# Optimization experiments

Hardware: AMD Instinct MI355X
Metric: run time of the kernel (lower is better)

## Reference

```python
import jax, jax.numpy as jnp
import numpy as np

TYPE_PANEL, TYPE_DIALOG, TYPE_CHAR = 1, 2, 3
NUM_ELEMS = 64  # max element index per type (panel count cap per page)
B, S, D = 8, 4096, 768
NPC, NDS = 4, 4  # num_panel_classes, num_dialog_shapes


def setup_inputs() -> dict:
    key = jax.random.key(0)
    ks = jax.random.split(key, 16)
    w = lambda k, shp: jax.random.normal(k, shp, dtype=jnp.float32) * 0.02
    return {
        "element_types": jax.random.randint(ks[0], (B, S), 0, 4, dtype=jnp.int32),
        "element_indices": jax.random.randint(ks[1], (B, S), 0, NUM_ELEMS, dtype=jnp.int32),
        "parent_panel_indices": jax.random.randint(ks[2], (B, S), 0, NUM_ELEMS, dtype=jnp.int32),
        "style_vector": jax.random.normal(ks[3], (B, 4), dtype=jnp.float32),
        "type_emb": w(ks[4], (4, D)),
        "index_emb": w(ks[5], (NUM_ELEMS, D)),
        "parent_emb": w(ks[6], (NUM_ELEMS, D)),
        "style_w": w(ks[7], (4, D)),
        "style_b": jnp.zeros((D,), jnp.float32),
        "ln_g": jnp.ones((D,), jnp.float32),
        "ln_b": jnp.zeros((D,), jnp.float32),
        "panel_w": w(ks[8], (D, NPC + 4)),
        "panel_b": jnp.zeros((NPC + 4,), jnp.float32),
        "dialog_w": w(ks[9], (2 * D, NDS + 4)),
        "dialog_b": jnp.zeros((NDS + 4,), jnp.float32),
        "char_w": w(ks[10], (2 * D, 4)),
        "char_b": jnp.zeros((4,), jnp.float32),
    }


def reference(element_types, element_indices, parent_panel_indices, style_vector,
              type_emb, index_emb, parent_emb, style_w, style_b, ln_g, ln_b,
              panel_w, panel_b, dialog_w, dialog_b, char_w, char_b):
    Bv, Sv = element_types.shape
    # --- TokenLayoutEncoder: embedding sum + style projection + LayerNorm ---
    x = type_emb[element_types] + index_emb[element_indices] + parent_emb[parent_panel_indices]
    x = x + (style_vector @ style_w + style_b)[:, None, :]
    mu = x.mean(-1, keepdims=True)
    var = ((x - mu) ** 2).mean(-1, keepdims=True)
    feats = (x - mu) * jax.lax.rsqrt(var + 1e-5) * ln_g + ln_b  # (B,S,D)

    # --- vectorized _build_parent_remap: orig panel idx -> kept panel order pos ---
    panel_mask = element_types == TYPE_PANEL                      # (B,S)
    kept = (jnp.cumsum(panel_mask, axis=1) - 1).astype(jnp.int32) # order pos of each panel token
    brow = jnp.arange(Bv, dtype=jnp.int32)[:, None]
    col = jnp.where(panel_mask, element_indices, NUM_ELEMS)       # dummy slot for non-panels
    remap = (jnp.full((Bv, NUM_ELEMS + 1), -1, jnp.int32)
             .at[brow, col].max(kept))[:, :NUM_ELEMS]             # (B, NUM_ELEMS)
    # kept panel order pos -> sequence position (for parent feature gather)
    slot = jnp.where(panel_mask, kept, Sv)
    seq_ids = jnp.broadcast_to(jnp.arange(Sv, dtype=jnp.int32), (Bv, Sv))
    pos_table = (jnp.zeros((Bv, Sv + 1), jnp.int32)
                 .at[brow, slot].set(seq_ids))[:, :Sv]            # (B,S)

    # --- parent_pos per token (DIALOG/CHAR only), -1 otherwise ---
    child_mask = (element_types == TYPE_DIALOG) | (element_types == TYPE_CHAR)
    ppos = jnp.where(child_mask,
                     jnp.take_along_axis(remap, parent_panel_indices, axis=1), -1)
    valid = ppos >= 0
    pseq = jnp.take_along_axis(pos_table, jnp.clip(ppos, 0, Sv - 1), axis=1)
    parent_feats = jnp.take_along_axis(feats, pseq[..., None], axis=1)
    parent_feats = parent_feats * valid[..., None].astype(feats.dtype)
    cat = jnp.concatenate([feats, parent_feats], axis=-1)         # (B,S,2D)

    # --- ParallelPredictionHeads, masked per token type ---
    panel_out = (feats @ panel_w + panel_b) * panel_mask[..., None].astype(feats.dtype)
    dmask = ((element_types == TYPE_DIALOG) & valid)[..., None].astype(feats.dtype)
    cmask = ((element_types == TYPE_CHAR) & valid)[..., None].astype(feats.dtype)
    dialog_out = (cat @ dialog_w + dialog_b) * dmask
    char_out = (cat @ char_w + char_b) * cmask
    return panel_out, dialog_out, char_out
```

## Files before the change

### kernel.cpp

```cpp
#include <hip/hip_runtime.h>

#define NB 8
#define NS 4096
#define ND 768

#define WPACK_F4 6528
#define LDS_F4   6720

typedef float4 f4;

static __device__ __forceinline__ f4 ld4(const float* __restrict__ p, int i) {
    return ((const f4*)p)[i];
}

static __device__ __forceinline__ void dot4(float& acc, const f4& a, const f4& w) {
    acc = fmaf(a.x, w.x, acc);
    acc = fmaf(a.y, w.y, acc);
    acc = fmaf(a.z, w.z, acc);
    acc = fmaf(a.w, w.w, acc);
}

__global__ __launch_bounds__(256) void lp_pre(
    const int* __restrict__ et, const int* __restrict__ ei,
    const float* __restrict__ sv, const float* __restrict__ sw,
    const float* __restrict__ sb,
    const float* __restrict__ pw, const float* __restrict__ dw,
    const float* __restrict__ cw,
    const float* __restrict__ lng, const float* __restrict__ lnb,
    int* __restrict__ table, float* __restrict__ sprj,
    float* __restrict__ wpack)
{
    const int bx = blockIdx.x;
    if (bx < 128) {
        int t = bx * 256 + threadIdx.x;
        if (et[t] == 1) {
            int b = t >> 12;
            atomicMax(&table[b * 64 + ei[t]], t & (NS - 1));
        }
    } else if (bx < 130) {
        const int lane = threadIdx.x & 63;
        const int b = (bx - 128) * 4 + (threadIdx.x >> 6);
        const float sv0 = sv[b*4+0], sv1 = sv[b*4+1], sv2 = sv[b*4+2], sv3 = sv[b*4+3];
        #pragma unroll
        for (int g = 0; g < 3; ++g) {
            int i = g*64 + lane;
            f4 w0 = ld4(sw, i), w1 = ld4(sw, 192+i), w2 = ld4(sw, 384+i), w3 = ld4(sw, 576+i);
            f4 bb = ld4(sb, i);
            f4 r;
            r.x = bb.x + sv0*w0.x + sv1*w1.x + sv2*w2.x + sv3*w3.x;
            r.y = bb.y + sv0*w0.y + sv1*w1.y + sv2*w2.y + sv3*w3.y;
            r.z = bb.z + sv0*w0.z + sv1*w1.z + sv2*w2.z + sv3*w3.z;
            r.w = bb.w + sv0*w0.w + sv1*w1.w + sv2*w2.w + sv3*w3.w;
            ((f4*)(sprj + b*ND))[i] = r;
        }
    } else {
        const int q = (bx - 130) * 256 + threadIdx.x;
        if (q >= WPACK_F4) return;
        f4 r;
        if (q < 1536) {
            int o = q / 192, i = q - o * 192, d0 = 4 * i;
            r.x = pw[(d0+0)*8 + o];
            r.y = pw[(d0+1)*8 + o];
            r.z = pw[(d0+2)*8 + o];
            r.w = pw[(d0+3)*8 + o];
        } else if (q < 4608) {
            int u = q - 1536;
            int o = u / 384, i = u - o * 384;
            int d0 = (i < 192) ? 4*i : 768 + 4*(i - 192);
            r.x = dw[(d0+0)*8 + o];
            r.y = dw[(d0+1)*8 + o];
            r.z = dw[(d0+2)*8 + o];
            r.w = dw[(d0+3)*8 + o];
        } else if (q < 6144) {
            int u = q - 4608;
            int o = u / 384, i = u - o * 384;
            int d0 = (i < 192) ? 4*i : 768 + 4*(i - 192);
            r.x = cw[(d0+0)*4 + o];
            r.y = cw[(d0+1)*4 + o];
            r.z = cw[(d0+2)*4 + o];
            r.w = cw[(d0+3)*4 + o];
        } else if (q < 6336) {
            r = ld4(lng, q - 6144);
        } else {
            r = ld4(lnb, q - 6336);
        }
        ((f4*)wpack)[q] = r;
    }
}

__global__ __launch_bounds__(256) void lp_parent(
    const int* __restrict__ ei, const int* __restrict__ ppi,
    const float* __restrict__ temb, const float* __restrict__ iemb,
    const float* __restrict__ pemb, const float* __restrict__ lng,
    const float* __restrict__ lnb,
    const int* __restrict__ table, const float* __restrict__ sprj,
    float* __restrict__ pfeat)
{
    const int lane = threadIdx.x & 63;
    const int slot = blockIdx.x * 4 + (threadIdx.x >> 6);
    const int b = slot >> 6;
    const int pp = table[slot];
    if (pp < 0) return;
    const int ptok = b * NS + pp;
    const int pei = ei[ptok], pppi = ppi[ptok];
    const float* ie = iemb + pei * ND;
    const float* pe = pemb + pppi * ND;
    const float* sp = sprj + b * ND;

    f4 x[3]; float s1 = 0.f, sq = 0.f;
    #pragma unroll
    for (int g = 0; g < 3; ++g) {
        int i = g*64 + lane;
        f4 a = ld4(temb + ND, i), c = ld4(ie, i), d = ld4(pe, i), s = ld4(sp, i);
        f4 v;
        v.x = a.x + c.x + d.x + s.x;
        v.y = a.y + c.y + d.y + s.y;
        v.z = a.z + c.z + d.z + s.z;
        v.w = a.w + c.w + d.w + s.w;
        x[g] = v;
        s1 += v.x + v.y + v.z + v.w;
        sq = fmaf(v.x, v.x, sq);
        sq = fmaf(v.y, v.y, sq);
        sq = fmaf(v.z, v.z, sq);
        sq = fmaf(v.w, v.w, sq);
    }
    #pragma unroll
    for (int k = 32; k >= 1; k >>= 1) {
        s1 += __shfl_xor(s1, k, 64);
        sq += __shfl_xor(sq, k, 64);
    }
    float mu = s1 * (1.f/ND);
    float rs = rsqrtf(sq * (1.f/ND) - mu * mu + 1e-5f);
    float c0 = -mu * rs;
    float* dst = pfeat + (size_t)slot * ND;
    #pragma unroll
    for (int g = 0; g < 3; ++g) {
        int i = g*64 + lane;
        f4 gg = ld4(lng, i), bb = ld4(lnb, i);
        f4 v = x[g], xn;
        xn.x = fmaf(v.x, rs, c0); v.x = fmaf(xn.x, gg.x, bb.x);
        xn.y = fmaf(v.y, rs, c0); v.y = fmaf(xn.y, gg.y, bb.y);
        xn.z = fmaf(v.z, rs, c0); v.z = fmaf(xn.z, gg.z, bb.z);
        xn.w = fmaf(v.w, rs, c0); v.w = fmaf(xn.w, gg.w, bb.w);
        ((f4*)dst)[i] = v;
    }
}

__global__ __launch_bounds__(1024) void lp_main(
    const int* __restrict__ et, const int* __restrict__ ei, const int* __restrict__ ppi,
    const float* __restrict__ temb, const float* __restrict__ iemb,
    const float* __restrict__ pemb,
    const float* __restrict__ pb, const float* __restrict__ db,
    const float* __restrict__ cb,
    const int* __restrict__ table, const float* __restrict__ sprj,
    const float* __restrict__ wpack, const float* __restrict__ pfeat,
    float* __restrict__ out)
{
    __shared__ f4 S[LDS_F4];
    const int tid = threadIdx.x;
    const int lane = tid & 63;
    const int wid = tid >> 6;
    const int t0 = blockIdx.x << 4;
    const int b = t0 >> 12;

    const f4* wsrc = (const f4*)wpack;
    for (int i = tid; i < WPACK_F4; i += 1024) S[i] = wsrc[i];
    if (tid < 192) S[WPACK_F4 + tid] = ((const f4*)(sprj + b * ND))[tid];
    __syncthreads();

    const int t = t0 + wid;
    const int type = et[t];

    f4 z4; z4.x = 0.f; z4.y = 0.f; z4.z = 0.f; z4.w = 0.f;
    f4 po0 = z4, po1 = z4, dq0 = z4, dq1 = z4, cq0 = z4;

    if (type != 0) {
        const int my_ei = ei[t], my_ppi = ppi[t];
        int pp = -1;
        if (type != 1) pp = table[b * 64 + my_ppi];

        const float* te = temb + type * ND;
        const float* ie = iemb + my_ei * ND;
        const float* pe = pemb + my_ppi * ND;

        f4 x[3];
        float s1 = 0.f, sq = 0.f;
        #pragma unroll
        for (int g = 0; g < 3; ++g) {
            int i = g * 64 + lane;
            f4 a = ld4(te, i), c = ld4(ie, i), d = ld4(pe, i);
            f4 s = S[WPACK_F4 + i];
            f4 v;
            v.x = a.x + c.x + d.x + s.x;
            v.y = a.y + c.y + d.y + s.y;
            v.z = a.z + c.z + d.z + s.z;
            v.w = a.w + c.w + d.w + s.w;
            x[g] = v;
            s1 += v.x + v.y + v.z + v.w;
            sq = fmaf(v.x, v.x, sq);
            sq = fmaf(v.y, v.y, sq);
            sq = fmaf(v.z, v.z, sq);
            sq = fmaf(v.w, v.w, sq);
        }
        #pragma unroll
        for (int k = 32; k >= 1; k >>= 1) {
            s1 += __shfl_xor(s1, k, 64);
            sq += __shfl_xor(sq, k, 64);
        }
        float mu = s1 * (1.f / ND);
        float rs = rsqrtf(sq * (1.f / ND) - mu * mu + 1e-5f);
        float c0 = -mu * rs;
        #pragma unroll
        for (int g = 0; g < 3; ++g) {
            int i = g * 64 + lane;
            f4 gg = S[6144 + i], bb = S[6336 + i];
            f4 v = x[g], xn;
            xn.x = fmaf(v.x, rs, c0); v.x = fmaf(xn.x, gg.x, bb.x);
            xn.y = fmaf(v.y, rs, c0); v.y = fmaf(xn.y, gg.y, bb.y);
            xn.z = fmaf(v.z, rs, c0); v.z = fmaf(xn.z, gg.z, bb.z);
            xn.w = fmaf(v.w, rs, c0); v.w = fmaf(xn.w, gg.w, bb.w);
            x[g] = v;
        }

        if (type == 1) {
            float acc[8];
            #pragma unroll
            for (int o = 0; o < 8; ++o) acc[o] = 0.f;
            #pragma unroll
            for (int g = 0; g < 3; ++g) {
                int i = g * 64 + lane;
                #pragma unroll
                for (int o = 0; o < 8; ++o)
                    dot4(acc[o], x[g], S[o * 192 + i]);
            }
            #pragma unroll
            for (int k = 32; k >= 1; k >>= 1) {
                #pragma unroll
                for (int o = 0; o < 8; ++o)
                    acc[o] += __shfl_xor(acc[o], k, 64);
            }
            po0.x = acc[0] + pb[0]; po0.y = acc[1] + pb[1];
            po0.z = acc[2] + pb[2]; po0.w = acc[3] + pb[3];
            po1.x = acc[4] + pb[4]; po1.y = acc[5] + pb[5];
            po1.z = acc[6] + pb[6]; po1.w = acc[7] + pb[7];
        } else if (pp >= 0) {
            const float* pfr = pfeat + (size_t)(b * 64 + my_ppi) * ND;
            if (type == 2) {
                float acc[8];
                #pragma unroll
                for (int o = 0; o < 8; ++o) acc[o] = 0.f;
                #pragma unroll
                for (int g = 0; g < 3; ++g) {
                    int i = g * 64 + lane;
                    #pragma unroll
                    for (int o = 0; o < 8; ++o)
                        dot4(acc[o], x[g], S[1536 + o * 384 + i]);
                }
                #pragma unroll
                for (int g = 0; g < 3; ++g)
                    x[g] = ld4(pfr, g * 64 + lane);
                #pragma unroll
                for (int g = 0; g < 3; ++g) {
                    int i = g * 64 + lane;
                    #pragma unroll
                    for (int o = 0; o < 8; ++o)
                        dot4(acc[o], x[g], S[1536 + o * 384 + 192 + i]);
                }
                #pragma unroll
                for (int k = 32; k >= 1; k >>= 1) {
                    #pragma unroll
                    for (int o = 0; o < 8; ++o)
                        acc[o] += __shfl_xor(acc[o], k, 64);
                }
                dq0.x = acc[0] + db[0]; dq0.y = acc[1] + db[1];
                dq0.z = acc[2] + db[2]; dq0.w = acc[3] + db[3];
                dq1.x = acc[4] + db[4]; dq1.y = acc[5] + db[5];
                dq1.z = acc[6] + db[6]; dq1.w = acc[7] + db[7];
            } else {
                float acc[4];
                #pragma unroll
                for (int o = 0; o < 4; ++o) acc[o] = 0.f;
                #pragma unroll
                for (int g = 0; g < 3; ++g) {
                    int i = g * 64 + lane;
                    #pragma unroll
                    for (int o = 0; o < 4; ++o)
                        dot4(acc[o], x[g], S[4608 + o * 384 + i]);
                }
                #pragma unroll
                for (int g = 0; g < 3; ++g)
                    x[g] = ld4(pfr, g * 64 + lane);
                #pragma unroll
                for (int g = 0; g < 3; ++g) {
                    int i = g * 64 + lane;
                    #pragma unroll
                    for (int o = 0; o < 4; ++o)
                        dot4(acc[o], x[g], S[4608 + o * 384 + 192 + i]);
                }
                #pragma unroll
                for (int k = 32; k >= 1; k >>= 1) {
                    #pragma unroll
                    for (int o = 0; o < 4; ++o)
                        acc[o] += __shfl_xor(acc[o], k, 64);
                }
                cq0.x = acc[0] + cb[0]; cq0.y = acc[1] + cb[1];
                cq0.z = acc[2] + cb[2]; cq0.w = acc[3] + cb[3];
            }
        }
    }

    if (lane == 0) {
        f4* op = (f4*)(out + (size_t)t * 8);
        op[0] = po0; op[1] = po1;
        f4* od = (f4*)(out + (size_t)NB * NS * 8 + (size_t)t * 8);
        od[0] = dq0; od[1] = dq1;
        ((f4*)(out + (size_t)NB * NS * 16 + (size_t)t * 4))[0] = cq0;
    }
}

extern "C" void kernel_launch(void* const* d_in, const int* in_sizes, int n_in,
                              void* d_out, int out_size, void* d_ws, size_t ws_size,
                              hipStream_t stream) {
    const int* et  = (const int*)d_in[0];
    const int* ei  = (const int*)d_in[1];
    const int* ppi = (const int*)d_in[2];
    const float* sv   = (const float*)d_in[3];
    const float* temb = (const float*)d_in[4];
    const float* iemb = (const float*)d_in[5];
    const float* pemb = (const float*)d_in[6];
    const float* sw   = (const float*)d_in[7];
    const float* sb   = (const float*)d_in[8];
    const float* lng  = (const float*)d_in[9];
    const float* lnb  = (const float*)d_in[10];
    const float* pw   = (const float*)d_in[11];
    const float* pb   = (const float*)d_in[12];
    const float* dw   = (const float*)d_in[13];
    const float* db   = (const float*)d_in[14];
    const float* cw   = (const float*)d_in[15];
    const float* cbp  = (const float*)d_in[16];
    float* out = (float*)d_out;

    int*   table = (int*)d_ws;
    float* sprj  = (float*)((char*)d_ws + 4096);
    float* wpack = (float*)((char*)d_ws + 32768);
    float* pfeat = (float*)((char*)d_ws + 32768 + WPACK_F4 * 16);

    hipMemsetAsync(table, 0xFF, NB * 64 * sizeof(int), stream);

    lp_pre<<<156, 256, 0, stream>>>(et, ei, sv, sw, sb, pw, dw, cw, lng, lnb,
                                    table, sprj, wpack);
    lp_parent<<<128, 256, 0, stream>>>(ei, ppi, temb, iemb, pemb, lng, lnb,
                                       table, sprj, pfeat);
    lp_main<<<(NB*NS)/16, 1024, 0, stream>>>(et, ei, ppi, temb, iemb, pemb,
                                             pb, db, cbp,
                                             table, sprj, wpack, pfeat, out);
}
```

Baseline: 145.1 us.

## Fuse memset, prepass, parent and main kernels into one cooperative persistent kernel

Merges the table memset, the weight-pack/style prepass, the parent-feature kernel and the main head kernel into a single cooperative launch of 256 blocks of 1024 threads, with grid-wide syncs between phases. Each block now handles 128 tokens in a loop instead of 16, so the roughly 100 KB packed-weight copy into LDS is amortised over eight times more tokens. This removes per-launch gaps and redundant LDS fills. The costs are three grid barriers and less parallel slack per block. If the cooperative launch fails, the code falls back to four ordinary launches of the same kernel.

```diff
diff --git a/kernel.cpp b/kernel.cpp
--- a/kernel.cpp
+++ b/kernel.cpp
@@ -1,4 +1,7 @@
 #include <hip/hip_runtime.h>
+#include <hip/hip_cooperative_groups.h>
+
+namespace cg = cooperative_groups;
 
 #define NB 8
 #define NS 4096
@@ -20,301 +23,299 @@
     acc = fmaf(a.w, w.w, acc);
 }
 
-__global__ __launch_bounds__(256) void lp_pre(
-    const int* __restrict__ et, const int* __restrict__ ei,
-    const float* __restrict__ sv, const float* __restrict__ sw,
-    const float* __restrict__ sb,
-    const float* __restrict__ pw, const float* __restrict__ dw,
-    const float* __restrict__ cw,
-    const float* __restrict__ lng, const float* __restrict__ lnb,
-    int* __restrict__ table, float* __restrict__ sprj,
-    float* __restrict__ wpack)
-{
-    const int bx = blockIdx.x;
-    if (bx < 128) {
-        int t = bx * 256 + threadIdx.x;
-        if (et[t] == 1) {
-            int b = t >> 12;
-            atomicMax(&table[b * 64 + ei[t]], t & (NS - 1));
-        }
-    } else if (bx < 130) {
-        const int lane = threadIdx.x & 63;
-        const int b = (bx - 128) * 4 + (threadIdx.x >> 6);
-        const float sv0 = sv[b*4+0], sv1 = sv[b*4+1], sv2 = sv[b*4+2], sv3 = sv[b*4+3];
-        #pragma unroll
-        for (int g = 0; g < 3; ++g) {
-            int i = g*64 + lane;
-            f4 w0 = ld4(sw, i), w1 = ld4(sw, 192+i), w2 = ld4(sw, 384+i), w3 = ld4(sw, 576+i);
-            f4 bb = ld4(sb, i);
-            f4 r;
-            r.x = bb.x + sv0*w0.x + sv1*w1.x + sv2*w2.x + sv3*w3.x;
-            r.y = bb.y + sv0*w0.y + sv1*w1.y + sv2*w2.y + sv3*w3.y;
-            r.z = bb.z + sv0*w0.z + sv1*w1.z + sv2*w2.z + sv3*w3.z;
-            r.w = bb.w + sv0*w0.w + sv1*w1.w + sv2*w2.w + sv3*w3.w;
-            ((f4*)(sprj + b*ND))[i] = r;
-        }
-    } else {
-        const int q = (bx - 130) * 256 + threadIdx.x;
-        if (q >= WPACK_F4) return;
-        f4 r;
-        if (q < 1536) {
-            int o = q / 192, i = q - o * 192, d0 = 4 * i;
-            r.x = pw[(d0+0)*8 + o];
-            r.y = pw[(d0+1)*8 + o];
-            r.z = pw[(d0+2)*8 + o];
-            r.w = pw[(d0+3)*8 + o];
-        } else if (q < 4608) {
-            int u = q - 1536;
-            int o = u / 384, i = u - o * 384;
-            int d0 = (i < 192) ? 4*i : 768 + 4*(i - 192);
-            r.x = dw[(d0+0)*8 + o];
-            r.y = dw[(d0+1)*8 + o];
-            r.z = dw[(d0+2)*8 + o];
-            r.w = dw[(d0+3)*8 + o];
-        } else if (q < 6144) {
-            int u = q - 4608;
-            int o = u / 384, i = u - o * 384;
-            int d0 = (i < 192) ? 4*i : 768 + 4*(i - 192);
-            r.x = cw[(d0+0)*4 + o];
-            r.y = cw[(d0+1)*4 + o];
-            r.z = cw[(d0+2)*4 + o];
-            r.w = cw[(d0+3)*4 + o];
-        } else if (q < 6336) {
-            r = ld4(lng, q - 6144);
-        } else {
-            r = ld4(lnb, q - 6336);
-        }
-        ((f4*)wpack)[q] = r;
-    }
-}
-
-__global__ __launch_bounds__(256) void lp_parent(
-    const int* __restrict__ ei, const int* __restrict__ ppi,
-    const float* __restrict__ temb, const float* __restrict__ iemb,
-    const float* __restrict__ pemb, const float* __restrict__ lng,
-    const float* __restrict__ lnb,
-    const int* __restrict__ table, const float* __restrict__ sprj,
-    float* __restrict__ pfeat)
-{
-    const int lane = threadIdx.x & 63;
-    const int slot = blockIdx.x * 4 + (threadIdx.x >> 6);
-    const int b = slot >> 6;
-    const int pp = table[slot];
-    if (pp < 0) return;
-    const int ptok = b * NS + pp;
-    const int pei = ei[ptok], pppi = ppi[ptok];
-    const float* ie = iemb + pei * ND;
-    const float* pe = pemb + pppi * ND;
-    const float* sp = sprj + b * ND;
-
-    f4 x[3]; float s1 = 0.f, sq = 0.f;
-    #pragma unroll
-    for (int g = 0; g < 3; ++g) {
-        int i = g*64 + lane;
-        f4 a = ld4(temb + ND, i), c = ld4(ie, i), d = ld4(pe, i), s = ld4(sp, i);
-        f4 v;
-        v.x = a.x + c.x + d.x + s.x;
-        v.y = a.y + c.y + d.y + s.y;
-        v.z = a.z + c.z + d.z + s.z;
-        v.w = a.w + c.w + d.w + s.w;
-        x[g] = v;
-        s1 += v.x + v.y + v.z + v.w;
-        sq = fmaf(v.x, v.x, sq);
-        sq = fmaf(v.y, v.y, sq);
-        sq = fmaf(v.z, v.z, sq);
-        sq = fmaf(v.w, v.w, sq);
-    }
-    #pragma unroll
-    for (int k = 32; k >= 1; k >>= 1) {
-        s1 += __shfl_xor(s1, k, 64);
-        sq += __shfl_xor(sq, k, 64);
-    }
-    float mu = s1 * (1.f/ND);
-    float rs = rsqrtf(sq * (1.f/ND) - mu * mu + 1e-5f);
-    float c0 = -mu * rs;
-    float* dst = pfeat + (size_t)slot * ND;
-    #pragma unroll
-    for (int g = 0; g < 3; ++g) {
-        int i = g*64 + lane;
-        f4 gg = ld4(lng, i), bb = ld4(lnb, i);
-        f4 v = x[g], xn;
-        xn.x = fmaf(v.x, rs, c0); v.x = fmaf(xn.x, gg.x, bb.x);
-        xn.y = fmaf(v.y, rs, c0); v.y = fmaf(xn.y, gg.y, bb.y);
-        xn.z = fmaf(v.z, rs, c0); v.z = fmaf(xn.z, gg.z, bb.z);
-        xn.w = fmaf(v.w, rs, c0); v.w = fmaf(xn.w, gg.w, bb.w);
-        ((f4*)dst)[i] = v;
-    }
-}
-
-__global__ __launch_bounds__(1024) void lp_main(
+__global__ __launch_bounds__(1024) void lp_all(
     const int* __restrict__ et, const int* __restrict__ ei, const int* __restrict__ ppi,
+    const float* __restrict__ sv,
     const float* __restrict__ temb, const float* __restrict__ iemb,
     const float* __restrict__ pemb,
-    const float* __restrict__ pb, const float* __restrict__ db,
-    const float* __restrict__ cb,
-    const int* __restrict__ table, const float* __restrict__ sprj,
-    const float* __restrict__ wpack, const float* __restrict__ pfeat,
-    float* __restrict__ out)
+    const float* __restrict__ sw, const float* __restrict__ sb,
+    const float* __restrict__ lng, const float* __restrict__ lnb,
+    const float* __restrict__ pw, const float* __restrict__ pb,
+    const float* __restrict__ dw, const float* __restrict__ db,
+    const float* __restrict__ cw, const float* __restrict__ cb,
+    int* __restrict__ table, float* __restrict__ sprj,
+    float* __restrict__ wpack, float* __restrict__ pfeat,
+    float* __restrict__ out, int mode)
 {
     __shared__ f4 S[LDS_F4];
     const int tid = threadIdx.x;
     const int lane = tid & 63;
     const int wid = tid >> 6;
-    const int t0 = blockIdx.x << 4;
-    const int b = t0 >> 12;
-
-    const f4* wsrc = (const f4*)wpack;
-    for (int i = tid; i < WPACK_F4; i += 1024) S[i] = wsrc[i];
-    if (tid < 192) S[WPACK_F4 + tid] = ((const f4*)(sprj + b * ND))[tid];
-    __syncthreads();
-
-    const int t = t0 + wid;
-    const int type = et[t];
-
-    f4 z4; z4.x = 0.f; z4.y = 0.f; z4.z = 0.f; z4.w = 0.f;
-    f4 po0 = z4, po1 = z4, dq0 = z4, dq1 = z4, cq0 = z4;
-
-    if (type != 0) {
-        const int my_ei = ei[t], my_ppi = ppi[t];
-        int pp = -1;
-        if (type != 1) pp = table[b * 64 + my_ppi];
-
-        const float* te = temb + type * ND;
-        const float* ie = iemb + my_ei * ND;
-        const float* pe = pemb + my_ppi * ND;
-
-        f4 x[3];
-        float s1 = 0.f, sq = 0.f;
-        #pragma unroll
-        for (int g = 0; g < 3; ++g) {
-            int i = g * 64 + lane;
-            f4 a = ld4(te, i), c = ld4(ie, i), d = ld4(pe, i);
-            f4 s = S[WPACK_F4 + i];
-            f4 v;
-            v.x = a.x + c.x + d.x + s.x;
-            v.y = a.y + c.y + d.y + s.y;
-            v.z = a.z + c.z + d.z + s.z;
-            v.w = a.w + c.w + d.w + s.w;
-            x[g] = v;
-            s1 += v.x + v.y + v.z + v.w;
-            sq = fmaf(v.x, v.x, sq);
-            sq = fmaf(v.y, v.y, sq);
-            sq = fmaf(v.z, v.z, sq);
-            sq = fmaf(v.w, v.w, sq);
+    const int bx = blockIdx.x;
+    const bool coop = (mode == 0);
+
+    if (coop || mode == 1) {
+        int q = bx * 1024 + tid;
+        if (q < WPACK_F4) {
+            f4 r;
+            if (q < 1536) {
+                int o = q / 192, i = q - o * 192, d0 = 4 * i;
+                r.x = pw[(d0+0)*8 + o];
+                r.y = pw[(d0+1)*8 + o];
+                r.z = pw[(d0+2)*8 + o];
+                r.w = pw[(d0+3)*8 + o];
+            } else if (q < 4608) {
+                int u = q - 1536;
+                int o = u / 384, i = u - o * 384;
+                int d0 = (i < 192) ? 4*i : 768 + 4*(i - 192);
+                r.x = dw[(d0+0)*8 + o];
+                r.y = dw[(d0+1)*8 + o];
+                r.z = dw[(d0+2)*8 + o];
+                r.w = dw[(d0+3)*8 + o];
+            } else if (q < 6144) {
+                int u = q - 4608;
+                int o = u / 384, i = u - o * 384;
+                int d0 = (i < 192) ? 4*i : 768 + 4*(i - 192);
+                r.x = cw[(d0+0)*4 + o];
+                r.y = cw[(d0+1)*4 + o];
+                r.z = cw[(d0+2)*4 + o];
+                r.w = cw[(d0+3)*4 + o];
+            } else if (q < 6336) {
+                r = ld4(lng, q - 6144);
+            } else {
+                r = ld4(lnb, q - 6336);
+            }
+            ((f4*)wpack)[q] = r;
+        } else if (q < WPACK_F4 + NB * 64) {
+            table[q - WPACK_F4] = -1;
         }
-        #pragma unroll
-        for (int k = 32; k >= 1; k >>= 1) {
-            s1 += __shfl_xor(s1, k, 64);
-            sq += __shfl_xor(sq, k, 64);
-        }
-        float mu = s1 * (1.f / ND);
-        float rs = rsqrtf(sq * (1.f / ND) - mu * mu + 1e-5f);
-        float c0 = -mu * rs;
-        #pragma unroll
-        for (int g = 0; g < 3; ++g) {
-            int i = g * 64 + lane;
-            f4 gg = S[6144 + i], bb = S[6336 + i];
-            f4 v = x[g], xn;
-            xn.x = fmaf(v.x, rs, c0); v.x = fmaf(xn.x, gg.x, bb.x);
-            xn.y = fmaf(v.y, rs, c0); v.y = fmaf(xn.y, gg.y, bb.y);
-            xn.z = fmaf(v.z, rs, c0); v.z = fmaf(xn.z, gg.z, bb.z);
-            xn.w = fmaf(v.w, rs, c0); v.w = fmaf(xn.w, gg.w, bb.w);
-            x[g] = v;
-        }
-
-        if (type == 1) {
-            float acc[8];
-            #pragma unroll
-            for (int o = 0; o < 8; ++o) acc[o] = 0.f;
+        if (bx == 7 && wid < 8) {
+            const int b = wid;
+            const float sv0 = sv[b*4+0], sv1 = sv[b*4+1], sv2 = sv[b*4+2], sv3 = sv[b*4+3];
             #pragma unroll
             for (int g = 0; g < 3; ++g) {
-                int i = g * 64 + lane;
-                #pragma unroll
-                for (int o = 0; o < 8; ++o)
-                    dot4(acc[o], x[g], S[o * 192 + i]);
-            }
-            #pragma unroll
-            for (int k = 32; k >= 1; k >>= 1) {
-                #pragma unroll
-                for (int o = 0; o < 8; ++o)
-                    acc[o] += __shfl_xor(acc[o], k, 64);
-            }
-            po0.x = acc[0] + pb[0]; po0.y = acc[1] + pb[1];
-            po0.z = acc[2] + pb[2]; po0.w = acc[3] + pb[3];
-            po1.x = acc[4] + pb[4]; po1.y = acc[5] + pb[5];
-            po1.z = acc[6] + pb[6]; po1.w = acc[7] + pb[7];
-        } else if (pp >= 0) {
-            const float* pfr = pfeat + (size_t)(b * 64 + my_ppi) * ND;
-            if (type == 2) {
-                float acc[8];
-                #pragma unroll
-                for (int o = 0; o < 8; ++o) acc[o] = 0.f;
+                int i = g*64 + lane;
+                f4 w0 = ld4(sw, i), w1 = ld4(sw, 192+i), w2 = ld4(sw, 384+i), w3 = ld4(sw, 576+i);
+                f4 bb = ld4(sb, i);
+                f4 r;
+                r.x = bb.x + sv0*w0.x + sv1*w1.x + sv2*w2.x + sv3*w3.x;
+                r.y = bb.y + sv0*w0.y + sv1*w1.y + sv2*w2.y + sv3*w3.y;
+                r.z = bb.z + sv0*w0.z + sv1*w1.z + sv2*w2.z + sv3*w3.z;
+                r.w = bb.w + sv0*w0.w + sv1*w1.w + sv2*w2.w + sv3*w3.w;
+                ((f4*)(sprj + b*ND))[i] = r;
+            }
+        }
+    }
+    if (coop) cg::this_grid().sync();
+
+    if (coop || mode == 2) {
+        int gt = bx * 1024 + tid;
+        if (gt < NB * NS && et[gt] == 1)
+            atomicMax(&table[(gt >> 12) * 64 + ei[gt]], gt & (NS - 1));
+    }
+    if (coop || mode >= 3) {
+        for (int i = tid; i < WPACK_F4; i += 1024) S[i] = ((const f4*)wpack)[i];
+        if (tid < 192) S[WPACK_F4 + tid] = ((const f4*)(sprj + (bx >> 5) * ND))[tid];
+        __syncthreads();
+    }
+    if (coop) cg::this_grid().sync();
+
+    if (coop || mode == 3) {
+        if (bx < 32) {
+            const int slot = bx * 16 + wid;
+            const int pp = table[slot];
+            if (pp >= 0) {
+                const int b = slot >> 6;
+                const int ptok = b * NS + pp;
+                const int pei = ei[ptok], pppi = ppi[ptok];
+                const float* ie = iemb + pei * ND;
+                const float* pe = pemb + pppi * ND;
+                const float* sp = sprj + b * ND;
+
+                f4 x[3]; float s1 = 0.f, sq = 0.f;
+                #pragma unroll
+                for (int g = 0; g < 3; ++g) {
+                    int i = g*64 + lane;
+                    f4 a = ld4(temb + ND, i), c = ld4(ie, i), d = ld4(pe, i), s = ld4(sp, i);
+                    f4 v;
+                    v.x = a.x + c.x + d.x + s.x;
+                    v.y = a.y + c.y + d.y + s.y;
+                    v.z = a.z + c.z + d.z + s.z;
+                    v.w = a.w + c.w + d.w + s.w;
+                    x[g] = v;
+                    s1 += v.x + v.y + v.z + v.w;
+                    sq = fmaf(v.x, v.x, sq);
+                    sq = fmaf(v.y, v.y, sq);
+                    sq = fmaf(v.z, v.z, sq);
+                    sq = fmaf(v.w, v.w, sq);
+                }
+                #pragma unroll
+                for (int k = 32; k >= 1; k >>= 1) {
+                    s1 += __shfl_xor(s1, k, 64);
+                    sq += __shfl_xor(sq, k, 64);
+                }
+                float mu = s1 * (1.f/ND);
+                float rs = rsqrtf(sq * (1.f/ND) - mu * mu + 1e-5f);
+                float c0 = -mu * rs;
+                float* dst = pfeat + (size_t)slot * ND;
+                #pragma unroll
+                for (int g = 0; g < 3; ++g) {
+                    int i = g*64 + lane;
+                    f4 gg = S[6144 + i], bb = S[6336 + i];
+                    f4 v = x[g], xn;
+                    xn.x = fmaf(v.x, rs, c0); v.x = fmaf(xn.x, gg.x, bb.x);
+                    xn.y = fmaf(v.y, rs, c0); v.y = fmaf(xn.y, gg.y, bb.y);
+                    xn.z = fmaf(v.z, rs, c0); v.z = fmaf(xn.z, gg.z, bb.z);
+                    xn.w = fmaf(v.w, rs, c0); v.w = fmaf(xn.w, gg.w, bb.w);
+                    ((f4*)dst)[i] = v;
+                }
+            }
+        }
+    }
+    if (coop) cg::this_grid().sync();
+
+    if (coop || mode == 4) {
+        const int b = bx >> 5;
+        for (int r = 0; r < 8; ++r) {
+            const int t = bx * 128 + r * 16 + wid;
+            const int type = et[t];
+
+            f4 z4; z4.x = 0.f; z4.y = 0.f; z4.z = 0.f; z4.w = 0.f;
+            f4 po0 = z4, po1 = z4, dq0 = z4, dq1 = z4, cq0 = z4;
+
+            if (type != 0) {
+                const int my_ei = ei[t], my_ppi = ppi[t];
+                int pp = -1;
+                if (type != 1) pp = table[b * 64 + my_ppi];
+
+                const float* te = temb + type * ND;
+                const float* ie = iemb + my_ei * ND;
+                const float* pe = pemb + my_ppi * ND;
+
+                f4 x[3];
+                float s1 = 0.f, sq = 0.f;
                 #pragma unroll
                 for (int g = 0; g < 3; ++g) {
                     int i = g * 64 + lane;
-                    #pragma unroll
-                    for (int o = 0; o < 8; ++o)
-                        dot4(acc[o], x[g], S[1536 + o * 384 + i]);
-                }
-                #pragma unroll
-                for (int g = 0; g < 3; ++g)
-                    x[g] = ld4(pfr, g * 64 + lane);
+                    f4 a = ld4(te, i), c = ld4(ie, i), d = ld4(pe, i);
+                    f4 s = S[WPACK_F4 + i];
+                    f4 v;
+                    v.x = a.x + c.x + d.x + s.x;
+                    v.y = a.y + c.y + d.y + s.y;
+                    v.z = a.z + c.z + d.z + s.z;
+                    v.w = a.w + c.w + d.w + s.w;
+                    x[g] = v;
+                    s1 += v.x + v.y + v.z + v.w;
+                    sq = fmaf(v.x, v.x, sq);
+                    sq = fmaf(v.y, v.y, sq);
+                    sq = fmaf(v.z, v.z, sq);
+                    sq = fmaf(v.w, v.w, sq);
+                }
+                #pragma unroll
+                for (int k = 32; k >= 1; k >>= 1) {
+                    s1 += __shfl_xor(s1, k, 64);
+                    sq += __shfl_xor(sq, k, 64);
+                }
+                float mu = s1 * (1.f / ND);
+                float rs = rsqrtf(sq * (1.f / ND) - mu * mu + 1e-5f);
+                float c0 = -mu * rs;
                 #pragma unroll
                 for (int g = 0; g < 3; ++g) {
                     int i = g * 64 + lane;
+                    f4 gg = S[6144 + i], bb = S[6336 + i];
+                    f4 v = x[g], xn;
+                    xn.x = fmaf(v.x, rs, c0); v.x = fmaf(xn.x, gg.x, bb.x);
+                    xn.y = fmaf(v.y, rs, c0); v.y = fmaf(xn.y, gg.y, bb.y);
+                    xn.z = fmaf(v.z, rs, c0); v.z = fmaf(xn.z, gg.z, bb.z);
+                    xn.w = fmaf(v.w, rs, c0); v.w = fmaf(xn.w, gg.w, bb.w);
+                    x[g] = v;
+                }
+
+                if (type == 1) {
+                    float acc[8];
                     #pragma unroll
-                    for (int o = 0; o < 8; ++o)
-                        dot4(acc[o], x[g], S[1536 + o * 384 + 192 + i]);
-                }
-                #pragma unroll
-                for (int k = 32; k >= 1; k >>= 1) {
+                    for (int o = 0; o < 8; ++o) acc[o] = 0.f;
                     #pragma unroll
-                    for (int o = 0; o < 8; ++o)
-                        acc[o] += __shfl_xor(acc[o], k, 64);
-                }
-                dq0.x = acc[0] + db[0]; dq0.y = acc[1] + db[1];
-                dq0.z = acc[2] + db[2]; dq0.w = acc[3] + db[3];
-                dq1.x = acc[4] + db[4]; dq1.y = acc[5] + db[5];
-                dq1.z = acc[6] + db[6]; dq1.w = acc[7] + db[7];
-            } else {
-                float acc[4];
-                #pragma unroll
-                for (int o = 0; o < 4; ++o) acc[o] = 0.f;
-                #pragma unroll
-                for (int g = 0; g < 3; ++g) {
-                    int i = g * 64 + lane;
+                    for (int g = 0; g < 3; ++g) {
+                        int i = g * 64 + lane;
+                        #pragma unroll
+                        for (int o = 0; o < 8; ++o)
+                            dot4(acc[o], x[g], S[o * 192 + i]);
+                    }
                     #pragma unroll
-                    for (int o = 0; o < 4; ++o)
-                        dot4(acc[o], x[g], S[4608 + o * 384 + i]);
-                }
-                #pragma unroll
-                for (int g = 0; g < 3; ++g)
-                    x[g] = ld4(pfr, g * 64 + lane);
-                #pragma unroll
-                for (int g = 0; g < 3; ++g) {
-                    int i = g * 64 + lane;
-                    #pragma unroll
-                    for (int o = 0; o < 4; ++o)
-                        dot4(acc[o], x[g], S[4608 + o * 384 + 192 + i]);
-                }
-                #pragma unroll
-                for (int k = 32; k >= 1; k >>= 1) {
-                    #pragma unroll
-                    for (int o = 0; o < 4; ++o)
-                        acc[o] += __shfl_xor(acc[o], k, 64);
-                }
-                cq0.x = acc[0] + cb[0]; cq0.y = acc[1] + cb[1];
-                cq0.z = acc[2] + cb[2]; cq0.w = acc[3] + cb[3];
+                    for (int k = 32; k >= 1; k >>= 1) {
+                        #pragma unroll
+                        for (int o = 0; o < 8; ++o)
+                            acc[o] += __shfl_xor(acc[o], k, 64);
+                    }
+                    po0.x = acc[0] + pb[0]; po0.y = acc[1] + pb[1];
+                    po0.z = acc[2] + pb[2]; po0.w = acc[3] + pb[3];
+                    po1.x = acc[4] + pb[4]; po1.y = acc[5] + pb[5];
+                    po1.z = acc[6] + pb[6]; po1.w = acc[7] + pb[7];
+                } else if (pp >= 0) {
+                    const float* pfr = pfeat + (size_t)(b * 64 + my_ppi) * ND;
+                    if (type == 2) {
+                        float acc[8];
+                        #pragma unroll
+                        for (int o = 0; o < 8; ++o) acc[o] = 0.f;
+                        #pragma unroll
+                        for (int g = 0; g < 3; ++g) {
+                            int i = g * 64 + lane;
+                            #pragma unroll
+                            for (int o = 0; o < 8; ++o)
+                                dot4(acc[o], x[g], S[1536 + o * 384 + i]);
+                        }
+                        #pragma unroll
+                        for (int g = 0; g < 3; ++g)
+                            x[g] = ld4(pfr, g * 64 + lane);
+                        #pragma unroll
+                        for (int g = 0; g < 3; ++g) {
+                            int i = g * 64 + lane;
+                            #pragma unroll
+                            for (int o = 0; o < 8; ++o)
+                                dot4(acc[o], x[g], S[1536 + o * 384 + 192 + i]);
+                        }
+                        #pragma unroll
+                        for (int k = 32; k >= 1; k >>= 1) {
+                            #pragma unroll
+                            for (int o = 0; o < 8; ++o)
+                                acc[o] += __shfl_xor(acc[o], k, 64);
+                        }
+                        dq0.x = acc[0] + db[0]; dq0.y = acc[1] + db[1];
+                        dq0.z = acc[2] + db[2]; dq0.w = acc[3] + db[3];
+                        dq1.x = acc[4] + db[4]; dq1.y = acc[5] + db[5];
+                        dq1.z = acc[6] + db[6]; dq1.w = acc[7] + db[7];
+                    } else {
+                        float acc[4];
+                        #pragma unroll
+                        for (int o = 0; o < 4; ++o) acc[o] = 0.f;
+                        #pragma unroll
+                        for (int g = 0; g < 3; ++g) {
+                            int i = g * 64 + lane;
+                            #pragma unroll
+                            for (int o = 0; o < 4; ++o)
+                                dot4(acc[o], x[g], S[4608 + o * 384 + i]);
+                        }
+                        #pragma unroll
+                        for (int g = 0; g < 3; ++g)
+                            x[g] = ld4(pfr, g * 64 + lane);
+                        #pragma unroll
+                        for (int g = 0; g < 3; ++g) {
+                            int i = g * 64 + lane;
+                            #pragma unroll
+                            for (int o = 0; o < 4; ++o)
+                                dot4(acc[o], x[g], S[4608 + o * 384 + 192 + i]);
+                        }
+                        #pragma unroll
+                        for (int k = 32; k >= 1; k >>= 1) {
+                            #pragma unroll
+                            for (int o = 0; o < 4; ++o)
+                                acc[o] += __shfl_xor(acc[o], k, 64);
+                        }
+                        cq0.x = acc[0] + cb[0]; cq0.y = acc[1] + cb[1];
+                        cq0.z = acc[2] + cb[2]; cq0.w = acc[3] + cb[3];
+                    }
+                }
+            }
+
+            if (lane == 0) {
+                f4* op = (f4*)(out + (size_t)t * 8);
+                op[0] = po0; op[1] = po1;
+                f4* od = (f4*)(out + (size_t)NB * NS * 8 + (size_t)t * 8);
+                od[0] = dq0; od[1] = dq1;
+                ((f4*)(out + (size_t)NB * NS * 16 + (size_t)t * 4))[0] = cq0;
             }
         }
-    }
-
-    if (lane == 0) {
-        f4* op = (f4*)(out + (size_t)t * 8);
-        op[0] = po0; op[1] = po1;
-        f4* od = (f4*)(out + (size_t)NB * NS * 8 + (size_t)t * 8);
-        od[0] = dq0; od[1] = dq1;
-        ((f4*)(out + (size_t)NB * NS * 16 + (size_t)t * 4))[0] = cq0;
     }
 }
 
@@ -345,13 +346,28 @@
     float* wpack = (float*)((char*)d_ws + 32768);
     float* pfeat = (float*)((char*)d_ws + 32768 + WPACK_F4 * 16);
 
-    hipMemsetAsync(table, 0xFF, NB * 64 * sizeof(int), stream);
-
-    lp_pre<<<156, 256, 0, stream>>>(et, ei, sv, sw, sb, pw, dw, cw, lng, lnb,
-                                    table, sprj, wpack);
-    lp_parent<<<128, 256, 0, stream>>>(ei, ppi, temb, iemb, pemb, lng, lnb,
-                                       table, sprj, pfeat);
-    lp_main<<<(NB*NS)/16, 1024, 0, stream>>>(et, ei, ppi, temb, iemb, pemb,
-                                             pb, db, cbp,
-                                             table, sprj, wpack, pfeat, out);
+    int mode = 0;
+    void* args[] = { (void*)&et, (void*)&ei, (void*)&ppi, (void*)&sv,
+                     (void*)&temb, (void*)&iemb, (void*)&pemb,
+                     (void*)&sw, (void*)&sb, (void*)&lng, (void*)&lnb,
+                     (void*)&pw, (void*)&pb, (void*)&dw, (void*)&db,
+                     (void*)&cw, (void*)&cbp,
+                     (void*)&table, (void*)&sprj, (void*)&wpack, (void*)&pfeat,
+                     (void*)&out, (void*)&mode };
+    hipError_t e = hipLaunchCooperativeKernel((void*)lp_all, dim3(256), dim3(1024),
+                                              args, 0, stream);
+    if (e != hipSuccess) {
+        lp_all<<<8,   1024, 0, stream>>>(et, ei, ppi, sv, temb, iemb, pemb, sw, sb,
+                                         lng, lnb, pw, pb, dw, db, cw, cbp,
+                                         table, sprj, wpack, pfeat, out, 1);
+        lp_all<<<32,  1024, 0, stream>>>(et, ei, ppi, sv, temb, iemb, pemb, sw, sb,
+                                         lng, lnb, pw, pb, dw, db, cw, cbp,
+                                         table, sprj, wpack, pfeat, out, 2);
+        lp_all<<<32,  1024, 0, stream>>>(et, ei, ppi, sv, temb, iemb, pemb, sw, sb,
+                                         lng, lnb, pw, pb, dw, db, cw, cbp,
+                                         table, sprj, wpack, pfeat, out, 3);
+        lp_all<<<256, 1024, 0, stream>>>(et, ei, ppi, sv, temb, iemb, pemb, sw, sb,
+                                         lng, lnb, pw, pb, dw, db, cw, cbp,
+                                         table, sprj, wpack, pfeat, out, 4);
+    }
 }
```

After: 225.0 us. 1.55x slower.

## Compact tokens into per-role lists and process them with role-specialized blocks

Applied to the files above, without the earlier changes.

The pre-pass now builds per-batch compacted lists of panel, dialog and char token positions using wave ballots and atomics. The main kernel runs a persistent grid of 512 blocks, each assigned to one role, and loads only that role's weights plus the LN params into LDS. Type-0 tokens and children without a valid parent are skipped, and the output is zero-filled with a memset instead. The table encoding shifts to s+1 so that a zero memset can initialise it. This removes wasted waves and divergence and shrinks LDS use, at the cost of an extra output memset, atomic-ordered lists and possible load imbalance across roles.

```diff
diff --git a/kernel.cpp b/kernel.cpp
--- a/kernel.cpp
+++ b/kernel.cpp
@@ -5,7 +5,8 @@
 #define ND 768
 
 #define WPACK_F4 6528
-#define LDS_F4   6720
+
+#define MAIN_LDS_F4 3648
 
 typedef float4 f4;
 
@@ -27,15 +28,29 @@
     const float* __restrict__ pw, const float* __restrict__ dw,
     const float* __restrict__ cw,
     const float* __restrict__ lng, const float* __restrict__ lnb,
-    int* __restrict__ table, float* __restrict__ sprj,
-    float* __restrict__ wpack)
+    int* __restrict__ table, int* __restrict__ cnt, int* __restrict__ lists,
+    float* __restrict__ sprj, float* __restrict__ wpack)
 {
     const int bx = blockIdx.x;
     if (bx < 128) {
-        int t = bx * 256 + threadIdx.x;
-        if (et[t] == 1) {
-            int b = t >> 12;
-            atomicMax(&table[b * 64 + ei[t]], t & (NS - 1));
+        const int lane = threadIdx.x & 63;
+        const int t = bx * 256 + threadIdx.x;
+        const int b = t >> 12;
+        const int s = t & (NS - 1);
+        const int type = et[t];
+        if (type == 1) atomicMax(&table[b * 64 + ei[t]], s + 1);
+        #pragma unroll
+        for (int role = 0; role < 3; ++role) {
+            const int want = (type == role + 1);
+            unsigned long long m = __ballot(want);
+            if (want) {
+                int ldr = __ffsll(m) - 1;
+                int base = 0;
+                if (lane == ldr) base = atomicAdd(&cnt[role * 8 + b], (int)__popcll(m));
+                base = __shfl(base, ldr, 64);
+                int pos = (int)__popcll(m & ((1ull << lane) - 1));
+                lists[(role * 8 + b) * 4096 + base + pos] = s;
+            }
         }
     } else if (bx < 130) {
         const int lane = threadIdx.x & 63;
@@ -99,7 +114,7 @@
     const int lane = threadIdx.x & 63;
     const int slot = blockIdx.x * 4 + (threadIdx.x >> 6);
     const int b = slot >> 6;
-    const int pp = table[slot];
+    const int pp = table[slot] - 1;
     if (pp < 0) return;
     const int ptok = b * NS + pp;
     const int pei = ei[ptok], pppi = ppi[ptok];
@@ -146,40 +161,53 @@
     }
 }
 
-__global__ __launch_bounds__(1024) void lp_main(
-    const int* __restrict__ et, const int* __restrict__ ei, const int* __restrict__ ppi,
+__global__ __launch_bounds__(1024, 8) void lp_main(
+    const int* __restrict__ ei, const int* __restrict__ ppi,
     const float* __restrict__ temb, const float* __restrict__ iemb,
     const float* __restrict__ pemb,
     const float* __restrict__ pb, const float* __restrict__ db,
     const float* __restrict__ cb,
-    const int* __restrict__ table, const float* __restrict__ sprj,
+    const int* __restrict__ table, const int* __restrict__ cnt,
+    const int* __restrict__ lists, const float* __restrict__ sprj,
     const float* __restrict__ wpack, const float* __restrict__ pfeat,
     float* __restrict__ out)
 {
-    __shared__ f4 S[LDS_F4];
+    __shared__ f4 S[MAIN_LDS_F4];
     const int tid = threadIdx.x;
     const int lane = tid & 63;
     const int wid = tid >> 6;
-    const int t0 = blockIdx.x << 4;
-    const int b = t0 >> 12;
+    const int bx = blockIdx.x;
+    const int b = bx >> 6;
+    const int r = bx & 63;
+
+    int role, ridx, nb, wbase, wcnt;
+    if (r < 16)      { role = 0; ridx = r;      nb = 16; wbase = 0;    wcnt = 1536; }
+    else if (r < 48) { role = 1; ridx = r - 16; nb = 32; wbase = 1536; wcnt = 3072; }
+    else             { role = 2; ridx = r - 48; nb = 16; wbase = 4608; wcnt = 1536; }
 
     const f4* wsrc = (const f4*)wpack;
-    for (int i = tid; i < WPACK_F4; i += 1024) S[i] = wsrc[i];
-    if (tid < 192) S[WPACK_F4 + tid] = ((const f4*)(sprj + b * ND))[tid];
+    for (int i = tid; i < wcnt; i += 1024) S[i] = wsrc[wbase + i];
+    if (tid < 384) S[3072 + tid] = wsrc[6144 + tid];
+    if (tid < 192) S[3456 + tid] = ((const f4*)(sprj + b * ND))[tid];
     __syncthreads();
 
-    const int t = t0 + wid;
-    const int type = et[t];
-
-    f4 z4; z4.x = 0.f; z4.y = 0.f; z4.z = 0.f; z4.w = 0.f;
-    f4 po0 = z4, po1 = z4, dq0 = z4, dq1 = z4, cq0 = z4;
-
-    if (type != 0) {
+    const int n = cnt[role * 8 + b];
+    const int* lst = lists + (role * 8 + b) * 4096;
+    const int tb = b * NS;
+    const int step = nb * 16;
+    const float* te = temb + (role + 1) * ND;
+
+    for (int i = ridx * 16 + wid; i < n; i += step) {
+        const int s = lst[i];
+        const int t = tb + s;
         const int my_ei = ei[t], my_ppi = ppi[t];
-        int pp = -1;
-        if (type != 1) pp = table[b * 64 + my_ppi];
-
-        const float* te = temb + type * ND;
+
+        int pp = 0;
+        if (role != 0) {
+            pp = table[b * 64 + my_ppi] - 1;
+            if (pp < 0) continue;
+        }
+
         const float* ie = iemb + my_ei * ND;
         const float* pe = pemb + my_ppi * ND;
 
@@ -187,14 +215,14 @@
         float s1 = 0.f, sq = 0.f;
         #pragma unroll
         for (int g = 0; g < 3; ++g) {
-            int i = g * 64 + lane;
-            f4 a = ld4(te, i), c = ld4(ie, i), d = ld4(pe, i);
-            f4 s = S[WPACK_F4 + i];
+            int ii = g * 64 + lane;
+            f4 a = ld4(te, ii), c = ld4(ie, ii), d = ld4(pe, ii);
+            f4 sp = S[3456 + ii];
             f4 v;
-            v.x = a.x + c.x + d.x + s.x;
-            v.y = a.y + c.y + d.y + s.y;
-            v.z = a.z + c.z + d.z + s.z;
-            v.w = a.w + c.w + d.w + s.w;
+            v.x = a.x + c.x + d.x + sp.x;
+            v.y = a.y + c.y + d.y + sp.y;
+            v.z = a.z + c.z + d.z + sp.z;
+            v.w = a.w + c.w + d.w + sp.w;
             x[g] = v;
             s1 += v.x + v.y + v.z + v.w;
             sq = fmaf(v.x, v.x, sq);
@@ -212,8 +240,8 @@
         float c0 = -mu * rs;
         #pragma unroll
         for (int g = 0; g < 3; ++g) {
-            int i = g * 64 + lane;
-            f4 gg = S[6144 + i], bb = S[6336 + i];
+            int ii = g * 64 + lane;
+            f4 gg = S[3072 + ii], bb = S[3264 + ii];
             f4 v = x[g], xn;
             xn.x = fmaf(v.x, rs, c0); v.x = fmaf(xn.x, gg.x, bb.x);
             xn.y = fmaf(v.y, rs, c0); v.y = fmaf(xn.y, gg.y, bb.y);
@@ -222,16 +250,16 @@
             x[g] = v;
         }
 
-        if (type == 1) {
+        if (role == 0) {
             float acc[8];
             #pragma unroll
             for (int o = 0; o < 8; ++o) acc[o] = 0.f;
             #pragma unroll
             for (int g = 0; g < 3; ++g) {
-                int i = g * 64 + lane;
+                int ii = g * 64 + lane;
                 #pragma unroll
                 for (int o = 0; o < 8; ++o)
-                    dot4(acc[o], x[g], S[o * 192 + i]);
+                    dot4(acc[o], x[g], S[o * 192 + ii]);
             }
             #pragma unroll
             for (int k = 32; k >= 1; k >>= 1) {
@@ -239,32 +267,37 @@
                 for (int o = 0; o < 8; ++o)
                     acc[o] += __shfl_xor(acc[o], k, 64);
             }
-            po0.x = acc[0] + pb[0]; po0.y = acc[1] + pb[1];
-            po0.z = acc[2] + pb[2]; po0.w = acc[3] + pb[3];
-            po1.x = acc[4] + pb[4]; po1.y = acc[5] + pb[5];
-            po1.z = acc[6] + pb[6]; po1.w = acc[7] + pb[7];
-        } else if (pp >= 0) {
+            if (lane == 0) {
+                f4 r0, r1;
+                r0.x = acc[0] + pb[0]; r0.y = acc[1] + pb[1];
+                r0.z = acc[2] + pb[2]; r0.w = acc[3] + pb[3];
+                r1.x = acc[4] + pb[4]; r1.y = acc[5] + pb[5];
+                r1.z = acc[6] + pb[6]; r1.w = acc[7] + pb[7];
+                f4* op = (f4*)(out + (size_t)t * 8);
+                op[0] = r0; op[1] = r1;
+            }
+        } else {
             const float* pfr = pfeat + (size_t)(b * 64 + my_ppi) * ND;
-            if (type == 2) {
+            if (role == 1) {
                 float acc[8];
                 #pragma unroll
                 for (int o = 0; o < 8; ++o) acc[o] = 0.f;
                 #pragma unroll
                 for (int g = 0; g < 3; ++g) {
-                    int i = g * 64 + lane;
+                    int ii = g * 64 + lane;
                     #pragma unroll
                     for (int o = 0; o < 8; ++o)
-                        dot4(acc[o], x[g], S[1536 + o * 384 + i]);
+                        dot4(acc[o], x[g], S[o * 384 + ii]);
                 }
                 #pragma unroll
                 for (int g = 0; g < 3; ++g)
                     x[g] = ld4(pfr, g * 64 + lane);
                 #pragma unroll
                 for (int g = 0; g < 3; ++g) {
-                    int i = g * 64 + lane;
+                    int ii = g * 64 + lane;
                     #pragma unroll
                     for (int o = 0; o < 8; ++o)
-                        dot4(acc[o], x[g], S[1536 + o * 384 + 192 + i]);
+                        dot4(acc[o], x[g], S[o * 384 + 192 + ii]);
                 }
                 #pragma unroll
                 for (int k = 32; k >= 1; k >>= 1) {
@@ -272,30 +305,35 @@
                     for (int o = 0; o < 8; ++o)
                         acc[o] += __shfl_xor(acc[o], k, 64);
                 }
-                dq0.x = acc[0] + db[0]; dq0.y = acc[1] + db[1];
-                dq0.z = acc[2] + db[2]; dq0.w = acc[3] + db[3];
-                dq1.x = acc[4] + db[4]; dq1.y = acc[5] + db[5];
-                dq1.z = acc[6] + db[6]; dq1.w = acc[7] + db[7];
+                if (lane == 0) {
+                    f4 r0, r1;
+                    r0.x = acc[0] + db[0]; r0.y = acc[1] + db[1];
+                    r0.z = acc[2] + db[2]; r0.w = acc[3] + db[3];
+                    r1.x = acc[4] + db[4]; r1.y = acc[5] + db[5];
+                    r1.z = acc[6] + db[6]; r1.w = acc[7] + db[7];
+                    f4* od = (f4*)(out + (size_t)NB * NS * 8 + (size_t)t * 8);
+                    od[0] = r0; od[1] = r1;
+                }
             } else {
                 float acc[4];
                 #pragma unroll
                 for (int o = 0; o < 4; ++o) acc[o] = 0.f;
                 #pragma unroll
                 for (int g = 0; g < 3; ++g) {
-                    int i = g * 64 + lane;
+                    int ii = g * 64 + lane;
                     #pragma unroll
                     for (int o = 0; o < 4; ++o)
-                        dot4(acc[o], x[g], S[4608 + o * 384 + i]);
+                        dot4(acc[o], x[g], S[o * 384 + ii]);
                 }
                 #pragma unroll
                 for (int g = 0; g < 3; ++g)
                     x[g] = ld4(pfr, g * 64 + lane);
                 #pragma unroll
                 for (int g = 0; g < 3; ++g) {
-                    int i = g * 64 + lane;
+                    int ii = g * 64 + lane;
                     #pragma unroll
                     for (int o = 0; o < 4; ++o)
-                        dot4(acc[o], x[g], S[4608 + o * 384 + 192 + i]);
+                        dot4(acc[o], x[g], S[o * 384 + 192 + ii]);
                 }
                 #pragma unroll
                 for (int k = 32; k >= 1; k >>= 1) {
@@ -303,18 +341,14 @@
                     for (int o = 0; o < 4; ++o)
                         acc[o] += __shfl_xor(acc[o], k, 64);
                 }
-                cq0.x = acc[0] + cb[0]; cq0.y = acc[1] + cb[1];
-                cq0.z = acc[2] + cb[2]; cq0.w = acc[3] + cb[3];
-            }
-        }
-    }
-
-    if (lane == 0) {
-        f4* op = (f4*)(out + (size_t)t * 8);
-        op[0] = po0; op[1] = po1;
-        f4* od = (f4*)(out + (size_t)NB * NS * 8 + (size_t)t * 8);
-        od[0] = dq0; od[1] = dq1;
-        ((f4*)(out + (size_t)NB * NS * 16 + (size_t)t * 4))[0] = cq0;
+                if (lane == 0) {
+                    f4 r0;
+                    r0.x = acc[0] + cb[0]; r0.y = acc[1] + cb[1];
+                    r0.z = acc[2] + cb[2]; r0.w = acc[3] + cb[3];
+                    ((f4*)(out + (size_t)NB * NS * 16 + (size_t)t * 4))[0] = r0;
+                }
+            }
+        }
     }
 }
 
@@ -341,17 +375,21 @@
     float* out = (float*)d_out;
 
     int*   table = (int*)d_ws;
+    int*   cnt   = (int*)((char*)d_ws + 2048);
     float* sprj  = (float*)((char*)d_ws + 4096);
     float* wpack = (float*)((char*)d_ws + 32768);
-    float* pfeat = (float*)((char*)d_ws + 32768 + WPACK_F4 * 16);
-
-    hipMemsetAsync(table, 0xFF, NB * 64 * sizeof(int), stream);
+    int*   lists = (int*)((char*)d_ws + 137216);
+    float* pfeat = (float*)((char*)d_ws + 532480);
+
+    hipMemsetAsync(d_ws, 0, 2144, stream);
+    hipMemsetAsync(d_out, 0, out_size, stream);
 
     lp_pre<<<156, 256, 0, stream>>>(et, ei, sv, sw, sb, pw, dw, cw, lng, lnb,
-                                    table, sprj, wpack);
+                                    table, cnt, lists, sprj, wpack);
     lp_parent<<<128, 256, 0, stream>>>(ei, ppi, temb, iemb, pemb, lng, lnb,
                                        table, sprj, pfeat);
-    lp_main<<<(NB*NS)/16, 1024, 0, stream>>>(et, ei, ppi, temb, iemb, pemb,
-                                             pb, db, cbp,
-                                             table, sprj, wpack, pfeat, out);
-}
+    lp_main<<<512, 1024, 0, stream>>>(ei, ppi, temb, iemb, pemb,
+                                      pb, db, cbp,
+                                      table, cnt, lists, sprj, wpack, pfeat,
+                                      out);
+}
```

Measured after the change: 155.7 us. 1.07x slower.
